# Optimization experiments

Hardware: AMD Instinct MI355X
Metric: run time of the kernel (lower is better)

Reference implementation:

```python
import jax, jax.numpy as jnp
import numpy as np
import math

D_MODEL, D_K, D_V, N_HEADS = 1024, 64, 64, 16
B, LQ, LK = 4, 2048, 2048
LN_EPS = 1e-5


def setup_inputs() -> dict:
    key = jax.random.key(0)
    ks = jax.random.split(key, 8)
    s = 1.0 / math.sqrt(D_MODEL)
    return {
        "input_Q": jax.random.normal(ks[0], (B, LQ, D_MODEL), jnp.float32),
        "input_K": jax.random.normal(ks[1], (B, LK, D_MODEL), jnp.float32),
        "input_V": jax.random.normal(ks[2], (B, LK, D_MODEL), jnp.float32),
        "attn_mask": jax.random.randint(ks[3], (B, LQ, LK), 0, 2).astype(bool),
        # weights stored as [in, out] (torch Linear applies x @ W.T)
        "W_Q": jax.random.normal(ks[4], (D_MODEL, N_HEADS * D_K), jnp.float32) * s,
        "W_K": jax.random.normal(ks[5], (D_MODEL, N_HEADS * D_K), jnp.float32) * s,
        "W_V": jax.random.normal(ks[6], (D_MODEL, N_HEADS * D_V), jnp.float32) * s,
        "W_fc": jax.random.normal(ks[7], (N_HEADS * D_V, D_MODEL), jnp.float32) * s,
    }


def reference(input_Q, input_K, input_V, attn_mask, W_Q, W_K, W_V, W_fc):
    b, lq, _ = input_Q.shape
    lk = input_K.shape[1]
    # projections -> [b, len, h, d] -> [b, h, len, d]
    Q = (input_Q @ W_Q).reshape(b, lq, N_HEADS, D_K).transpose(0, 2, 1, 3)
    K = (input_K @ W_K).reshape(b, lk, N_HEADS, D_K).transpose(0, 2, 1, 3)
    V = (input_V @ W_V).reshape(b, lk, N_HEADS, D_V).transpose(0, 2, 1, 3)
    # scaled scores [b, h, q, k]
    scores = jnp.einsum("bhqd,bhkd->bhqk", Q, K) / math.sqrt(D_K)
    scores = jnp.where(attn_mask[:, None, :, :], -1e9, scores)
    attn = jax.nn.softmax(scores, axis=-1)
    # context [b, h, q, dv] -> [b, q, h*dv]
    ctx = jnp.einsum("bhqk,bhkd->bhqd", attn, V)
    ctx = ctx.transpose(0, 2, 1, 3).reshape(b, lq, N_HEADS * D_V)
    result = ctx @ W_fc
    x = result + input_Q
    mu = jnp.mean(x, axis=-1, keepdims=True)
    var = jnp.var(x, axis=-1, keepdims=True)
    res = (x - mu) / jnp.sqrt(var + LN_EPS)
    return res, attn
```

## Files before the change

### kernel.cpp

```cpp
#include <hip/hip_runtime.h>
#include <hip/hip_bf16.h>
#include <stdint.h>

#define DEVI __device__ __forceinline__

typedef __attribute__((ext_vector_type(8))) short bf16x8;
typedef __attribute__((ext_vector_type(4))) float f32x4;
typedef __attribute__((ext_vector_type(4))) unsigned u32x4;

static DEVI unsigned short f2bf(float f) {
  unsigned int u = __builtin_bit_cast(unsigned int, f);
  u = (u + 0x7FFFu + ((u >> 16) & 1u)) >> 16;
  return (unsigned short)u;
}

static DEVI void async16(const void* g, void* l) {
  __builtin_amdgcn_global_load_lds((__attribute__((address_space(1))) void*)(g),
                                   (__attribute__((address_space(3))) void*)(l),
                                   16, 0, 0);
}

__global__ __launch_bounds__(256) void cvt_kernel(const float* __restrict__ in,
                                                  unsigned short* __restrict__ out, int n4) {
  int i = blockIdx.x * 256 + threadIdx.x;
  if (i >= n4) return;
  float4 v = ((const float4*)in)[i];
  uint2 o;
  o.x = (unsigned)f2bf(v.x) | ((unsigned)f2bf(v.y) << 16);
  o.y = (unsigned)f2bf(v.z) | ((unsigned)f2bf(v.w) << 16);
  ((uint2*)out)[i] = o;
}

__global__ __launch_bounds__(256) void maskbits_kernel(const int* __restrict__ mask,
                                                       unsigned long long* __restrict__ mb) {
  size_t tg = (size_t)blockIdx.x * 256 + threadIdx.x;
  int v = mask[tg];
  unsigned long long bal = __ballot(v != 0);
  if ((threadIdx.x & 63) == 0) mb[tg >> 6] = bal;
}

__global__ __launch_bounds__(256) void wtrans_kernel(const float* __restrict__ W,
                                                     unsigned short* __restrict__ Wt,
                                                     float scale) {
  __shared__ float t[32][33];
  const int bx = blockIdx.x * 32;
  const int by = blockIdx.y * 32;
  const int tx = threadIdx.x, ty = threadIdx.y;
#pragma unroll
  for (int i = 0; i < 32; i += 8) t[ty + i][tx] = W[(size_t)(by + ty + i) * 1024 + bx + tx];
  __syncthreads();
#pragma unroll
  for (int i = 0; i < 32; i += 8)
    Wt[(size_t)(bx + ty + i) * 1024 + by + tx] = f2bf(t[tx][ty + i] * scale);
}

template <bool OUT_F32>
__global__ __launch_bounds__(256) void gemm_nt(const unsigned short* __restrict__ A, int lda,
                                               const unsigned short* __restrict__ B, int ldb,
                                               void* __restrict__ Cp, int ldc, int K) {
  __shared__ unsigned short As[128 * 64];
  __shared__ unsigned short Bs[128 * 64];
  const int tid = threadIdx.x;
  const int wave = tid >> 6, lane = tid & 63;
  const int m0 = blockIdx.x * 128, n0 = blockIdx.y * 128;
  const int wr = (wave >> 1) * 64, wc = (wave & 1) * 64;
  const int fr = lane & 15, fg = lane >> 4;
  f32x4 acc[4][4] = {};
  for (int kt = 0; kt < K; kt += 64) {
    __syncthreads();
#pragma unroll
    for (int it = 0; it < 4; ++it) {
      int id = it * 256 + tid;
      int row = id >> 3, ch = id & 7;
      async16(A + (size_t)(m0 + row) * lda + kt + ch * 8,
              (char*)As + (it * 256 + wave * 64) * 16);
      async16(B + (size_t)(n0 + row) * ldb + kt + ch * 8,
              (char*)Bs + (it * 256 + wave * 64) * 16);
    }
    __syncthreads();
#pragma unroll
    for (int ks = 0; ks < 2; ++ks) {
      bf16x8 af[4], bfr[4];
#pragma unroll
      for (int i = 0; i < 4; ++i)
        af[i] = *(const bf16x8*)(As + (wr + i * 16 + fr) * 64 + ks * 32 + fg * 8);
#pragma unroll
      for (int j = 0; j < 4; ++j)
        bfr[j] = *(const bf16x8*)(Bs + (wc + j * 16 + fr) * 64 + ks * 32 + fg * 8);
#pragma unroll
      for (int i = 0; i < 4; ++i)
#pragma unroll
        for (int j = 0; j < 4; ++j)
          acc[i][j] = __builtin_amdgcn_mfma_f32_16x16x32_bf16(af[i], bfr[j], acc[i][j], 0, 0, 0);
    }
  }
#pragma unroll
  for (int i = 0; i < 4; ++i)
#pragma unroll
    for (int j = 0; j < 4; ++j)
#pragma unroll
      for (int r = 0; r < 4; ++r) {
        int row = m0 + wr + i * 16 + fg * 4 + r;
        int col = n0 + wc + j * 16 + fr;
        if (OUT_F32)
          ((float*)Cp)[(size_t)row * ldc + col] = acc[i][j][r];
        else
          ((unsigned short*)Cp)[(size_t)row * ldc + col] = f2bf(acc[i][j][r]);
      }
}

__global__ __launch_bounds__(256) void vtrans_kernel(const unsigned short* __restrict__ Vp,
                                                     unsigned short* __restrict__ Vt) {
  __shared__ unsigned short t[64][72];
  const int bh = blockIdx.y;
  const int b = bh >> 4, h = bh & 15;
  const int l0 = blockIdx.x * 64;
  const int tid = threadIdx.x;
#pragma unroll
  for (int it = 0; it < 2; ++it) {
    int id = it * 256 + tid;
    int l = id >> 3, ch = id & 7;
    uint4 v = *(const uint4*)(Vp + (size_t)(b * 2048 + l0 + l) * 1024 + h * 64 + ch * 8);
    *(uint4*)(&t[l][ch * 8]) = v;
  }
  __syncthreads();
#pragma unroll
  for (int it = 0; it < 2; ++it) {
    int id = it * 256 + tid;
    int d = id >> 3, lc = id & 7;
    unsigned short o[8];
#pragma unroll
    for (int k = 0; k < 8; ++k) o[k] = t[lc * 8 + k][d];
    uint4 ov;
    ov.x = o[0] | ((unsigned)o[1] << 16);
    ov.y = o[2] | ((unsigned)o[3] << 16);
    ov.z = o[4] | ((unsigned)o[5] << 16);
    ov.w = o[6] | ((unsigned)o[7] << 16);
    *(uint4*)(Vt + ((size_t)bh * 64 + d) * 2048 + l0 + lc * 8) = ov;
  }
}

__global__ __launch_bounds__(512, 4) void attn_kernel(
    const unsigned short* __restrict__ Qp, const unsigned short* __restrict__ Kp,
    const unsigned short* __restrict__ Vt, const unsigned long long* __restrict__ mb,
    float* __restrict__ attn_out, unsigned short* __restrict__ ctx) {
  __shared__ unsigned short Ks[2][4096];
  __shared__ unsigned short Vs[2][4096];
  __shared__ float Os[8][16 * 65];
  const int tid = threadIdx.x, wave = tid >> 6, lane = tid & 63;
  const int g = blockIdx.x;
  const int idx = g >> 3;
  const int bh = (g & 7) * 8 + (idx >> 4);
  const int b = bh >> 4, h = bh & 15;
  const int q0 = (idx & 15) * 128;
  const int fr = lane & 15, fg = lane >> 4;
  const int q = q0 + wave * 16 + fr;

  const int r0 = tid >> 3;
  const int chs = ((tid & 7) ^ (r0 & 7)) << 3;
  const unsigned short* kg = Kp + (size_t)(b * 2048 + r0) * 1024 + h * 64 + chs;
  const unsigned short* vg = Vt + (size_t)bh * 131072 + (size_t)r0 * 2048 + chs;

#define STAGE_K(buf, t) async16(kg + (size_t)(t) * 65536, (char*)Ks[buf] + wave * 1024)
#define STAGE_V(buf, t) async16(vg + (t) * 64, (char*)Vs[buf] + wave * 1024)

  const int c0 = (fg ^ (fr & 7)) << 3;
  const int c1 = ((4 + fg) ^ (fr & 7)) << 3;

  const unsigned short* qbase = Qp + (size_t)(b * 2048 + q) * 1024 + h * 64 + fg * 8;
  bf16x8 qa0 = *(const bf16x8*)(qbase);
  bf16x8 qa1 = *(const bf16x8*)(qbase + 32);

  const unsigned long long* mrow = mb + (size_t)(b * 2048 + q) * 32;
  const int msh = fg * 4;
  const float ninf = __uint_as_float(0xFF800000u);

  STAGE_K(0, 0);
  int cur = 0;
  float rsum = 0.f;
  for (int kt = 0; kt < 32; ++kt) {
    unsigned long long mw = mrow[kt];
    STAGE_K(cur ^ 1, (kt + 1) & 31);
    asm volatile("s_waitcnt vmcnt(2)" ::: "memory");
    __builtin_amdgcn_s_barrier();
    f32x4 s[4] = {};
#pragma unroll
    for (int j = 0; j < 4; ++j) {
      bf16x8 k0 = *(const bf16x8*)(&Ks[cur][(j * 16 + fr) * 64 + c0]);
      bf16x8 k1 = *(const bf16x8*)(&Ks[cur][(j * 16 + fr) * 64 + c1]);
      s[j] = __builtin_amdgcn_mfma_f32_16x16x32_bf16(k0, qa0, s[j], 0, 0, 0);
      s[j] = __builtin_amdgcn_mfma_f32_16x16x32_bf16(k1, qa1, s[j], 0, 0, 0);
    }
    unsigned mlo = (unsigned)mw, mhi = (unsigned)(mw >> 32);
#pragma unroll
    for (int j = 0; j < 4; ++j) {
      unsigned mj = ((j & 2) ? mhi : mlo) >> ((j & 1) * 16 + msh);
#pragma unroll
      for (int r = 0; r < 4; ++r) rsum += exp2f((mj & (1u << r)) ? ninf : s[j][r]);
    }
    asm volatile("s_waitcnt lgkmcnt(0)" ::: "memory");
    __builtin_amdgcn_s_barrier();
    cur ^= 1;
  }
  rsum += __shfl_xor(rsum, 16);
  rsum += __shfl_xor(rsum, 32);
  const float rs = 1.0f / rsum;

  STAGE_V(cur, 0);
  asm volatile("s_waitcnt vmcnt(0)" ::: "memory");
  __builtin_amdgcn_s_barrier();
  f32x4 o[4] = {};
  const int orow = lane >> 4, ocol = (lane & 15) * 4;
  float* abase = attn_out + ((size_t)bh * 2048 + q0 + wave * 16) * 2048;

  for (int kt = 0; kt < 32; ++kt) {
    unsigned long long mw = mrow[kt];
    STAGE_K(cur ^ 1, (kt + 1) & 31);
    STAGE_V(cur ^ 1, (kt + 1) & 31);
    asm volatile("s_waitcnt vmcnt(7)" ::: "memory");
    __builtin_amdgcn_s_barrier();
    f32x4 s[4] = {};
#pragma unroll
    for (int j = 0; j < 4; ++j) {
      bf16x8 k0 = *(const bf16x8*)(&Ks[cur][(j * 16 + fr) * 64 + c0]);
      bf16x8 k1 = *(const bf16x8*)(&Ks[cur][(j * 16 + fr) * 64 + c1]);
      s[j] = __builtin_amdgcn_mfma_f32_16x16x32_bf16(k0, qa0, s[j], 0, 0, 0);
      s[j] = __builtin_amdgcn_mfma_f32_16x16x32_bf16(k1, qa1, s[j], 0, 0, 0);
    }
    unsigned mlo = (unsigned)mw, mhi = (unsigned)(mw >> 32);
    unsigned pk[4][2];
#pragma unroll
    for (int j = 0; j < 4; ++j) {
      unsigned mj = ((j & 2) ? mhi : mlo) >> ((j & 1) * 16 + msh);
      float e0 = exp2f((mj & 1u) ? ninf : s[j][0]) * rs;
      float e1 = exp2f((mj & 2u) ? ninf : s[j][1]) * rs;
      float e2 = exp2f((mj & 4u) ? ninf : s[j][2]) * rs;
      float e3 = exp2f((mj & 8u) ? ninf : s[j][3]) * rs;
      f32x4 ev;
      ev[0] = e0; ev[1] = e1; ev[2] = e2; ev[3] = e3;
      *(f32x4*)(&Os[wave][fr * 65 + j * 16 + fg * 4]) = ev;
      asm("v_cvt_pk_bf16_f32 %0, %1, %2" : "=v"(pk[j][0]) : "v"(e0), "v"(e1));
      asm("v_cvt_pk_bf16_f32 %0, %1, %2" : "=v"(pk[j][1]) : "v"(e2), "v"(e3));
    }
    unsigned x0 = pk[0][0], y0 = pk[1][0], x1 = pk[0][1], y1 = pk[1][1];
    unsigned x2 = pk[2][0], y2 = pk[3][0], x3 = pk[2][1], y3 = pk[3][1];
    asm("v_permlane32_swap_b32 %0, %1" : "+v"(x0), "+v"(y0));
    asm("v_permlane16_swap_b32 %0, %1" : "+v"(x0), "+v"(y0));
    asm("v_permlane32_swap_b32 %0, %1" : "+v"(x1), "+v"(y1));
    asm("v_permlane16_swap_b32 %0, %1" : "+v"(x1), "+v"(y1));
    asm("v_permlane32_swap_b32 %0, %1" : "+v"(x2), "+v"(y2));
    asm("v_permlane16_swap_b32 %0, %1" : "+v"(x2), "+v"(y2));
    asm("v_permlane32_swap_b32 %0, %1" : "+v"(x3), "+v"(y3));
    asm("v_permlane16_swap_b32 %0, %1" : "+v"(x3), "+v"(y3));
    u32x4 t0, t1;
    t0[0] = x0; t0[1] = x1; t0[2] = y0; t0[3] = y1;
    t1[0] = x2; t1[1] = x3; t1[2] = y2; t1[3] = y3;
    bf16x8 pa0 = __builtin_bit_cast(bf16x8, t0);
    bf16x8 pa1 = __builtin_bit_cast(bf16x8, t1);
#pragma unroll
    for (int ct = 0; ct < 4; ++ct) {
      bf16x8 v0 = *(const bf16x8*)(&Vs[cur][(ct * 16 + fr) * 64 + c0]);
      bf16x8 v1 = *(const bf16x8*)(&Vs[cur][(ct * 16 + fr) * 64 + c1]);
      o[ct] = __builtin_amdgcn_mfma_f32_16x16x32_bf16(pa0, v0, o[ct], 0, 0, 0);
      o[ct] = __builtin_amdgcn_mfma_f32_16x16x32_bf16(pa1, v1, o[ct], 0, 0, 0);
    }
#pragma unroll
    for (int i = 0; i < 4; ++i) {
      f32x4 ov = *(const f32x4*)(&Os[wave][(orow + 4 * i) * 65 + ocol]);
      __builtin_nontemporal_store(
          ov, (f32x4*)(abase + (size_t)(orow + 4 * i) * 2048 + kt * 64 + ocol));
    }
    asm volatile("s_waitcnt lgkmcnt(0)" ::: "memory");
    __builtin_amdgcn_s_barrier();
    cur ^= 1;
  }
#pragma unroll
  for (int ct = 0; ct < 4; ++ct)
#pragma unroll
    for (int r = 0; r < 4; ++r)
      ctx[(size_t)(b * 2048 + q0 + wave * 16 + fg * 4 + r) * 1024 + h * 64 + ct * 16 + fr] =
          f2bf(o[ct][r]);
#undef STAGE_K
#undef STAGE_V
}

__global__ __launch_bounds__(256) void ln_kernel(const float* __restrict__ resl,
                                                 const float* __restrict__ inQ,
                                                 float* __restrict__ out) {
  __shared__ float red[8];
  const int row = blockIdx.x, tid = threadIdx.x;
  const int wave = tid >> 6, lane = tid & 63;
  float4 xv = ((const float4*)(resl + (size_t)row * 1024))[tid];
  float4 qv = ((const float4*)(inQ + (size_t)row * 1024))[tid];
  float v0 = xv.x + qv.x, v1 = xv.y + qv.y, v2 = xv.z + qv.z, v3 = xv.w + qv.w;
  float s = v0 + v1 + v2 + v3;
  float s2 = v0 * v0 + v1 * v1 + v2 * v2 + v3 * v3;
#pragma unroll
  for (int off = 1; off < 64; off <<= 1) {
    s += __shfl_xor(s, off);
    s2 += __shfl_xor(s2, off);
  }
  if (lane == 0) { red[wave] = s; red[4 + wave] = s2; }
  __syncthreads();
  s = red[0] + red[1] + red[2] + red[3];
  s2 = red[4] + red[5] + red[6] + red[7];
  const float mu = s * (1.0f / 1024.0f);
  const float var = s2 * (1.0f / 1024.0f) - mu * mu;
  const float inv = rsqrtf(var + 1e-5f);
  float4 ov;
  ov.x = (v0 - mu) * inv;
  ov.y = (v1 - mu) * inv;
  ov.z = (v2 - mu) * inv;
  ov.w = (v3 - mu) * inv;
  ((float4*)(out + (size_t)row * 1024))[tid] = ov;
}

extern "C" void kernel_launch(void* const* d_in, const int* in_sizes, int n_in, void* d_out,
                              int out_size, void* d_ws, size_t ws_size, hipStream_t stream) {
  const float* inQ = (const float*)d_in[0];
  const float* inK = (const float*)d_in[1];
  const float* inV = (const float*)d_in[2];
  const int* mask = (const int*)d_in[3];
  const float* WQ = (const float*)d_in[4];
  const float* WK = (const float*)d_in[5];
  const float* WV = (const float*)d_in[6];
  const float* WF = (const float*)d_in[7];
  float* res = (float*)d_out;
  float* attn = res + (size_t)8192 * 1024;

  char* w = (char*)d_ws;
  unsigned short* inQb = (unsigned short*)w; w += (size_t)16777216;
  unsigned short* inKb = (unsigned short*)w; w += (size_t)16777216;
  unsigned short* inVb = (unsigned short*)w; w += (size_t)16777216;
  unsigned short* WQt = (unsigned short*)w; w += (size_t)2097152;
  unsigned short* WKt = (unsigned short*)w; w += (size_t)2097152;
  unsigned short* WVt = (unsigned short*)w; w += (size_t)2097152;
  unsigned short* WFt = (unsigned short*)w; w += (size_t)2097152;
  unsigned short* Qp  = (unsigned short*)w; w += (size_t)16777216;
  unsigned short* Kp  = (unsigned short*)w; w += (size_t)16777216;
  unsigned short* Vp  = (unsigned short*)w; w += (size_t)16777216;
  unsigned short* Vtb = (unsigned short*)w; w += (size_t)16777216;
  unsigned short* ctx = (unsigned short*)w; w += (size_t)16777216;
  float* resl = (float*)w; w += (size_t)33554432;
  unsigned long long* mbits = (unsigned long long*)inQb;

  cvt_kernel<<<8192, 256, 0, stream>>>(inQ, inQb, 2097152);
  cvt_kernel<<<8192, 256, 0, stream>>>(inK, inKb, 2097152);
  cvt_kernel<<<8192, 256, 0, stream>>>(inV, inVb, 2097152);
  dim3 wb(32, 8);
  wtrans_kernel<<<dim3(32, 32), wb, 0, stream>>>(WQ, WQt, 0.18033688f);
  wtrans_kernel<<<dim3(32, 32), wb, 0, stream>>>(WK, WKt, 1.0f);
  wtrans_kernel<<<dim3(32, 32), wb, 0, stream>>>(WV, WVt, 1.0f);
  wtrans_kernel<<<dim3(32, 32), wb, 0, stream>>>(WF, WFt, 1.0f);
  gemm_nt<false><<<dim3(64, 8), 256, 0, stream>>>(inQb, 1024, WQt, 1024, Qp, 1024, 1024);
  gemm_nt<false><<<dim3(64, 8), 256, 0, stream>>>(inKb, 1024, WKt, 1024, Kp, 1024, 1024);
  gemm_nt<false><<<dim3(64, 8), 256, 0, stream>>>(inVb, 1024, WVt, 1024, Vp, 1024, 1024);
  maskbits_kernel<<<65536, 256, 0, stream>>>(mask, mbits);
  vtrans_kernel<<<dim3(32, 64), 256, 0, stream>>>(Vp, Vtb);
  attn_kernel<<<1024, 512, 0, stream>>>(Qp, Kp, Vtb, mbits, attn, ctx);
  gemm_nt<true><<<dim3(64, 8), 256, 0, stream>>>(ctx, 1024, WFt, 1024, resl, 1024, 1024);
  ln_kernel<<<8192, 256, 0, stream>>>(resl, inQ, res);
}
```

Measured before the change: 485.4 us.

## Process two K tiles per pass-1 iteration and remap GEMM blocks per XCD

The attention kernel's first pass (row-sum of exponentials) now stages and processes two 64-key tiles per iteration from a unified shared-memory buffer. This halves the number of barriers and wait points in that pass and loads the mask as 128-bit pairs. The GEMM kernels switch to a 1D grid whose block index is remapped so that blocks sharing A rows land on the same XCD, aiming for better L2 reuse. Shared memory is merged into one manually partitioned array, which keeps the footprint similar but adds address-arithmetic complexity.

```diff
diff --git a/kernel.cpp b/kernel.cpp
--- a/kernel.cpp
+++ b/kernel.cpp
@@ -62,7 +62,10 @@
   __shared__ unsigned short Bs[128 * 64];
   const int tid = threadIdx.x;
   const int wave = tid >> 6, lane = tid & 63;
-  const int m0 = blockIdx.x * 128, n0 = blockIdx.y * 128;
+  const int g = blockIdx.x;
+  const int xcd = g & 7, i4 = g >> 3;
+  const int m0 = (xcd * 8 + (i4 >> 3)) * 128;
+  const int n0 = (i4 & 7) * 128;
   const int wr = (wave >> 1) * 64, wc = (wave & 1) * 64;
   const int fr = lane & 15, fg = lane >> 4;
   f32x4 acc[4][4] = {};
@@ -144,9 +147,7 @@
     const unsigned short* __restrict__ Qp, const unsigned short* __restrict__ Kp,
     const unsigned short* __restrict__ Vt, const unsigned long long* __restrict__ mb,
     float* __restrict__ attn_out, unsigned short* __restrict__ ctx) {
-  __shared__ unsigned short Ks[2][4096];
-  __shared__ unsigned short Vs[2][4096];
-  __shared__ float Os[8][16 * 65];
+  __shared__ __align__(16) char smem[66048];
   const int tid = threadIdx.x, wave = tid >> 6, lane = tid & 63;
   const int g = blockIdx.x;
   const int idx = g >> 3;
@@ -161,8 +162,14 @@
   const unsigned short* kg = Kp + (size_t)(b * 2048 + r0) * 1024 + h * 64 + chs;
   const unsigned short* vg = Vt + (size_t)bh * 131072 + (size_t)r0 * 2048 + chs;
 
-#define STAGE_K(buf, t) async16(kg + (size_t)(t) * 65536, (char*)Ks[buf] + wave * 1024)
-#define STAGE_V(buf, t) async16(vg + (t) * 64, (char*)Vs[buf] + wave * 1024)
+#define STAGE_P1(buf, pair)                                                 \
+  do {                                                                      \
+    const unsigned short* _k = kg + (size_t)(pair) * 131072;                \
+    async16(_k, smem + (buf) * 16384 + wave * 1024);                        \
+    async16(_k + 65536, smem + (buf) * 16384 + 8192 + wave * 1024);         \
+  } while (0)
+#define STAGE_K2(buf, t) async16(kg + (size_t)(t) * 65536, smem + (buf) * 8192 + wave * 1024)
+#define STAGE_V2(buf, t) async16(vg + (t) * 64, smem + 16384 + (buf) * 8192 + wave * 1024)
 
   const int c0 = (fg ^ (fr & 7)) << 3;
   const int c1 = ((4 + fg) ^ (fr & 7)) << 3;
@@ -175,55 +182,75 @@
   const int msh = fg * 4;
   const float ninf = __uint_as_float(0xFF800000u);
 
-  STAGE_K(0, 0);
-  int cur = 0;
+#define P1_TILE(Kbase, mw)                                                       \
+  {                                                                              \
+    f32x4 s[4] = {};                                                             \
+    _Pragma("unroll") for (int j = 0; j < 4; ++j) {                              \
+      bf16x8 k0 = *(const bf16x8*)((Kbase) + (j * 16 + fr) * 64 + c0);           \
+      bf16x8 k1 = *(const bf16x8*)((Kbase) + (j * 16 + fr) * 64 + c1);           \
+      s[j] = __builtin_amdgcn_mfma_f32_16x16x32_bf16(k0, qa0, s[j], 0, 0, 0);    \
+      s[j] = __builtin_amdgcn_mfma_f32_16x16x32_bf16(k1, qa1, s[j], 0, 0, 0);    \
+    }                                                                            \
+    unsigned mlo = (unsigned)(mw), mhi = (unsigned)((mw) >> 32);                 \
+    _Pragma("unroll") for (int j = 0; j < 4; ++j) {                              \
+      unsigned mj = ((j & 2) ? mhi : mlo) >> ((j & 1) * 16 + msh);               \
+      _Pragma("unroll") for (int r = 0; r < 4; ++r)                              \
+          rsum += exp2f((mj & (1u << r)) ? ninf : s[j][r]);                      \
+    }                                                                            \
+  }
+
+  STAGE_P1(0, 0);
   float rsum = 0.f;
-  for (int kt = 0; kt < 32; ++kt) {
-    unsigned long long mw = mrow[kt];
-    STAGE_K(cur ^ 1, (kt + 1) & 31);
-    asm volatile("s_waitcnt vmcnt(2)" ::: "memory");
-    __builtin_amdgcn_s_barrier();
-    f32x4 s[4] = {};
-#pragma unroll
-    for (int j = 0; j < 4; ++j) {
-      bf16x8 k0 = *(const bf16x8*)(&Ks[cur][(j * 16 + fr) * 64 + c0]);
-      bf16x8 k1 = *(const bf16x8*)(&Ks[cur][(j * 16 + fr) * 64 + c1]);
-      s[j] = __builtin_amdgcn_mfma_f32_16x16x32_bf16(k0, qa0, s[j], 0, 0, 0);
-      s[j] = __builtin_amdgcn_mfma_f32_16x16x32_bf16(k1, qa1, s[j], 0, 0, 0);
-    }
-    unsigned mlo = (unsigned)mw, mhi = (unsigned)(mw >> 32);
-#pragma unroll
-    for (int j = 0; j < 4; ++j) {
-      unsigned mj = ((j & 2) ? mhi : mlo) >> ((j & 1) * 16 + msh);
-#pragma unroll
-      for (int r = 0; r < 4; ++r) rsum += exp2f((mj & (1u << r)) ? ninf : s[j][r]);
-    }
+  int buf = 0;
+  for (int kt2 = 0; kt2 < 15; ++kt2) {
+    ulonglong2 mp = *(const ulonglong2*)(mrow + 2 * kt2);
+    STAGE_P1(buf ^ 1, kt2 + 1);
+    asm volatile("s_waitcnt vmcnt(3)" ::: "memory");
+    __builtin_amdgcn_s_barrier();
+    const unsigned short* Ka = (const unsigned short*)(smem + buf * 16384);
+    P1_TILE(Ka, mp.x)
+    P1_TILE(Ka + 4096, mp.y)
     asm volatile("s_waitcnt lgkmcnt(0)" ::: "memory");
     __builtin_amdgcn_s_barrier();
-    cur ^= 1;
+    buf ^= 1;
+  }
+  {
+    ulonglong2 mp = *(const ulonglong2*)(mrow + 30);
+    asm volatile("s_waitcnt vmcnt(1)" ::: "memory");
+    __builtin_amdgcn_s_barrier();
+    const unsigned short* Ka = (const unsigned short*)(smem + buf * 16384);
+    P1_TILE(Ka, mp.x)
+    P1_TILE(Ka + 4096, mp.y)
+    asm volatile("s_waitcnt lgkmcnt(0)" ::: "memory");
+    __builtin_amdgcn_s_barrier();
   }
   rsum += __shfl_xor(rsum, 16);
   rsum += __shfl_xor(rsum, 32);
   const float rs = 1.0f / rsum;
 
-  STAGE_V(cur, 0);
+  STAGE_K2(0, 0);
+  STAGE_V2(0, 0);
   asm volatile("s_waitcnt vmcnt(0)" ::: "memory");
   __builtin_amdgcn_s_barrier();
   f32x4 o[4] = {};
   const int orow = lane >> 4, ocol = (lane & 15) * 4;
   float* abase = attn_out + ((size_t)bh * 2048 + q0 + wave * 16) * 2048;
+  float* Osw = (float*)(smem + 32768) + wave * 1040;
+  int cur = 0;
 
   for (int kt = 0; kt < 32; ++kt) {
     unsigned long long mw = mrow[kt];
-    STAGE_K(cur ^ 1, (kt + 1) & 31);
-    STAGE_V(cur ^ 1, (kt + 1) & 31);
+    STAGE_K2(cur ^ 1, (kt + 1) & 31);
+    STAGE_V2(cur ^ 1, (kt + 1) & 31);
     asm volatile("s_waitcnt vmcnt(7)" ::: "memory");
     __builtin_amdgcn_s_barrier();
+    const unsigned short* Kc = (const unsigned short*)(smem + cur * 8192);
+    const unsigned short* Vc = (const unsigned short*)(smem + 16384 + cur * 8192);
     f32x4 s[4] = {};
 #pragma unroll
     for (int j = 0; j < 4; ++j) {
-      bf16x8 k0 = *(const bf16x8*)(&Ks[cur][(j * 16 + fr) * 64 + c0]);
-      bf16x8 k1 = *(const bf16x8*)(&Ks[cur][(j * 16 + fr) * 64 + c1]);
+      bf16x8 k0 = *(const bf16x8*)(Kc + (j * 16 + fr) * 64 + c0);
+      bf16x8 k1 = *(const bf16x8*)(Kc + (j * 16 + fr) * 64 + c1);
       s[j] = __builtin_amdgcn_mfma_f32_16x16x32_bf16(k0, qa0, s[j], 0, 0, 0);
       s[j] = __builtin_amdgcn_mfma_f32_16x16x32_bf16(k1, qa1, s[j], 0, 0, 0);
     }
@@ -238,7 +265,7 @@
       float e3 = exp2f((mj & 8u) ? ninf : s[j][3]) * rs;
       f32x4 ev;
       ev[0] = e0; ev[1] = e1; ev[2] = e2; ev[3] = e3;
-      *(f32x4*)(&Os[wave][fr * 65 + j * 16 + fg * 4]) = ev;
+      *(f32x4*)(&Osw[fr * 65 + j * 16 + fg * 4]) = ev;
       asm("v_cvt_pk_bf16_f32 %0, %1, %2" : "=v"(pk[j][0]) : "v"(e0), "v"(e1));
       asm("v_cvt_pk_bf16_f32 %0, %1, %2" : "=v"(pk[j][1]) : "v"(e2), "v"(e3));
     }
@@ -259,14 +286,14 @@
     bf16x8 pa1 = __builtin_bit_cast(bf16x8, t1);
 #pragma unroll
     for (int ct = 0; ct < 4; ++ct) {
-      bf16x8 v0 = *(const bf16x8*)(&Vs[cur][(ct * 16 + fr) * 64 + c0]);
-      bf16x8 v1 = *(const bf16x8*)(&Vs[cur][(ct * 16 + fr) * 64 + c1]);
+      bf16x8 v0 = *(const bf16x8*)(Vc + (ct * 16 + fr) * 64 + c0);
+      bf16x8 v1 = *(const bf16x8*)(Vc + (ct * 16 + fr) * 64 + c1);
       o[ct] = __builtin_amdgcn_mfma_f32_16x16x32_bf16(pa0, v0, o[ct], 0, 0, 0);
       o[ct] = __builtin_amdgcn_mfma_f32_16x16x32_bf16(pa1, v1, o[ct], 0, 0, 0);
     }
 #pragma unroll
     for (int i = 0; i < 4; ++i) {
-      f32x4 ov = *(const f32x4*)(&Os[wave][(orow + 4 * i) * 65 + ocol]);
+      f32x4 ov = *(const f32x4*)(&Osw[(orow + 4 * i) * 65 + ocol]);
       __builtin_nontemporal_store(
           ov, (f32x4*)(abase + (size_t)(orow + 4 * i) * 2048 + kt * 64 + ocol));
     }
@@ -280,8 +307,10 @@
     for (int r = 0; r < 4; ++r)
       ctx[(size_t)(b * 2048 + q0 + wave * 16 + fg * 4 + r) * 1024 + h * 64 + ct * 16 + fr] =
           f2bf(o[ct][r]);
-#undef STAGE_K
-#undef STAGE_V
+#undef STAGE_P1
+#undef STAGE_K2
+#undef STAGE_V2
+#undef P1_TILE
 }
 
 __global__ __launch_bounds__(256) void ln_kernel(const float* __restrict__ resl,
@@ -352,12 +381,12 @@
   wtrans_kernel<<<dim3(32, 32), wb, 0, stream>>>(WK, WKt, 1.0f);
   wtrans_kernel<<<dim3(32, 32), wb, 0, stream>>>(WV, WVt, 1.0f);
   wtrans_kernel<<<dim3(32, 32), wb, 0, stream>>>(WF, WFt, 1.0f);
-  gemm_nt<false><<<dim3(64, 8), 256, 0, stream>>>(inQb, 1024, WQt, 1024, Qp, 1024, 1024);
-  gemm_nt<false><<<dim3(64, 8), 256, 0, stream>>>(inKb, 1024, WKt, 1024, Kp, 1024, 1024);
-  gemm_nt<false><<<dim3(64, 8), 256, 0, stream>>>(inVb, 1024, WVt, 1024, Vp, 1024, 1024);
+  gemm_nt<false><<<512, 256, 0, stream>>>(inQb, 1024, WQt, 1024, Qp, 1024, 1024);
+  gemm_nt<false><<<512, 256, 0, stream>>>(inKb, 1024, WKt, 1024, Kp, 1024, 1024);
+  gemm_nt<false><<<512, 256, 0, stream>>>(inVb, 1024, WVt, 1024, Vp, 1024, 1024);
   maskbits_kernel<<<65536, 256, 0, stream>>>(mask, mbits);
   vtrans_kernel<<<dim3(32, 64), 256, 0, stream>>>(Vp, Vtb);
   attn_kernel<<<1024, 512, 0, stream>>>(Qp, Kp, Vtb, mbits, attn, ctx);
-  gemm_nt<true><<<dim3(64, 8), 256, 0, stream>>>(ctx, 1024, WFt, 1024, resl, 1024, 1024);
+  gemm_nt<true><<<512, 256, 0, stream>>>(ctx, 1024, WFt, 1024, resl, 1024, 1024);
   ln_kernel<<<8192, 256, 0, stream>>>(resl, inQ, res);
 }
```

Result: slower. 568.1 us (+17.0%).
